# Kernel tuning notes

Measured on AMD Instinct MI355X. Metric: run time of the kernel, lower is better.

The kernel has to match this reference:

```python
import jax, jax.numpy as jnp
import numpy as np

# e2m1 (nvfp4) representable magnitudes and rounding midpoints
E2M1_POS = jnp.array([0.0, 0.5, 1.0, 1.5, 2.0, 3.0, 4.0, 6.0], dtype=jnp.float32)
E2M1_BOUNDS = jnp.array([0.25, 0.75, 1.25, 1.75, 2.5, 3.5, 5.0], dtype=jnp.float32)
E2M1_TABLE = jnp.concatenate([E2M1_POS, -E2M1_POS])  # 4-bit code -> value (sign bit = bit 3)
BLOCK = 16  # nvfp4 block-scale group size


def _fp8_round(v):
    # simulate storage of block scales in float8 e4m3
    return v.astype(jnp.float8_e4m3fn).astype(jnp.float32)


def _e2m1_round(v):
    # round-to-nearest onto the e2m1 grid (|v| must be pre-clipped to <= 6)
    idx = jnp.searchsorted(E2M1_BOUNDS, jnp.abs(v))
    return jnp.sign(v) * E2M1_POS[idx]


def setup_inputs() -> dict:
    key = jax.random.key(0)
    k1, k2, k3, k4, k5 = jax.random.split(key, 5)
    M, H = 4096, 4096
    x = jax.random.normal(k1, (M, 2 * H), dtype=jnp.float32)
    w = jax.random.randint(k2, (H, H // 2), 0, 256, dtype=jnp.int32)  # packed fp4, 2 nibbles/byte
    wscale = jax.random.normal(k3, (H, H // BLOCK), dtype=jnp.float32)  # cast to fp8 inside
    wscale2 = jax.random.uniform(k4, (1,), dtype=jnp.float32)
    scale = jax.random.uniform(k5, (1,), dtype=jnp.float32)
    return {"x": x, "w": w, "wscale": wscale, "wscale2": wscale2, "scale": scale}


def reference(x, w, wscale, wscale2, scale):
    M = x.shape[0]
    H = x.shape[1] // 2
    # SiLU-and-mul
    y = jax.nn.silu(x[:, :H]) * x[:, H:]                 # [M, H]
    gs = 1.0 / scale[0]                                  # global input scale (1/self.scale)
    # NVFP4 dynamic quant: per-16-element block amax -> fp8 block scale, values -> e2m1
    yb = y.reshape(M, H // BLOCK, BLOCK)
    amax = jnp.max(jnp.abs(yb), axis=-1)                 # [M, H/16]
    sf = _fp8_round(amax * (gs / 6.0))                   # fp8-stored block scales
    inv = jnp.where(sf > 0, gs / sf, 0.0)
    q = _e2m1_round(jnp.clip(yb * inv[..., None], -6.0, 6.0))
    a_deq = (q * sf[..., None]).reshape(M, H)            # fp4 value * fp8 block scale
    # Weight side: unpack fp4 nibbles (low nibble = even k), dequant with fp8 block scales
    wu = w.astype(jnp.uint8)
    lo = (wu & 0xF).astype(jnp.int32)
    hi = (wu >> 4).astype(jnp.int32)
    codes = jnp.stack([lo, hi], axis=-1).reshape(H, H)   # [N, K]
    b_q = E2M1_TABLE[codes]
    ws = _fp8_round(wscale)                              # model stores wscale in fp8
    b_deq = b_q * jnp.repeat(ws, BLOCK, axis=1)          # [N, K]
    # cutlass_scaled_fp4_mm with alpha = scale * wscale2 undoing global scales
    alpha = scale[0] * wscale2[0]
    out = alpha * (a_deq @ b_deq.T)                      # [M, N]
    return out
```

## Files before the change

kernel.cpp:

```cpp
#include <hip/hip_runtime.h>
#include <math.h>

typedef unsigned int uint;
typedef unsigned short ushort;
typedef __attribute__((ext_vector_type(8))) short bf16x8;
typedef __attribute__((ext_vector_type(4))) float f32x4;

static constexpr int Mdim = 4096;
static constexpr int Ndim = 4096;
static constexpr int Kdim = 4096;
static constexpr int Hdim = 4096;


__device__ __forceinline__ float fp8_round(float v) {
  float a = fabsf(v);
  float q;
  if (a >= 0x1p-6f) {
    uint u = __float_as_uint(a);
    int e = (int)(u >> 23) - 127;
    float quant = __uint_as_float((uint)(e - 3 + 127) << 23);
    q = rintf(a / quant) * quant;
    q = fminf(q, 448.f);
  } else {
    q = rintf(a * 512.f) * 0x1p-9f;
  }
  return copysignf(q, v);
}

__device__ __forceinline__ float e2m1_round(float t) {
  float a = fabsf(t);
  float q;
  if (a <= 0.25f) q = 0.f;
  else if (a <= 0.75f) q = 0.5f;
  else if (a <= 1.25f) q = 1.f;
  else if (a <= 1.75f) q = 1.5f;
  else if (a <= 2.5f)  q = 2.f;
  else if (a <= 3.5f)  q = 3.f;
  else if (a <= 5.f)   q = 4.f;
  else                 q = 6.f;
  return copysignf(q, t);
}

__device__ __forceinline__ float e2m1_decode(uint c) {
  uint m = c & 7u;
  float v;
  if (m == 0u) v = 0.f;
  else if (m == 1u) v = 0.5f;
  else v = __uint_as_float(((126u + (m >> 1)) << 23) | ((m & 1u) << 22));
  return (c & 8u) ? -v : v;
}


__global__ void silu_quant_kernel(const float* __restrict__ x, ushort* __restrict__ a_deq,
                                  const float* __restrict__ scalep) {
  const int g = blockIdx.x * 256 + threadIdx.x;
  const int row = g >> 8;
  const int blk = g & 255;
  const float gs = 1.0f / scalep[0];
  const float c6 = gs / 6.0f;
  const float* gp = x + (size_t)row * (2 * Hdim) + blk * 16;
  const float* up = gp + Hdim;
  float y[16];
  float amax = 0.f;
#pragma unroll
  for (int i = 0; i < 4; ++i) {
    float4 gv = ((const float4*)gp)[i];
    float4 uv = ((const float4*)up)[i];
    float ga[4] = {gv.x, gv.y, gv.z, gv.w};
    float ua[4] = {uv.x, uv.y, uv.z, uv.w};
#pragma unroll
    for (int j = 0; j < 4; ++j) {
      float xv = ga[j];
      float sig = 1.0f / (1.0f + expf(-xv));
      float yy = xv * sig * ua[j];
      y[i * 4 + j] = yy;
      amax = fmaxf(amax, fabsf(yy));
    }
  }
  const float sf = fp8_round(amax * c6);
  uint outp[8];
  if (sf > 0.f) {
    const float inv = gs / sf;
#pragma unroll
    for (int i = 0; i < 8; ++i) {
      float t0 = fminf(fmaxf(y[2 * i] * inv, -6.f), 6.f);
      float t1 = fminf(fmaxf(y[2 * i + 1] * inv, -6.f), 6.f);
      float d0 = e2m1_round(t0) * sf;
      float d1 = e2m1_round(t1) * sf;
      outp[i] = (__float_as_uint(d0) >> 16) | ((__float_as_uint(d1) >> 16) << 16);
    }
  } else {
#pragma unroll
    for (int i = 0; i < 8; ++i) outp[i] = 0u;
  }
  uint4* dst = (uint4*)(a_deq + (size_t)row * Hdim + blk * 16);
  dst[0] = (uint4){outp[0], outp[1], outp[2], outp[3]};
  dst[1] = (uint4){outp[4], outp[5], outp[6], outp[7]};
}


__global__ void wdeq_kernel(const int* __restrict__ w, const float* __restrict__ wscale,
                            ushort* __restrict__ b_deq) {
  const int g = blockIdx.x * 256 + threadIdx.x;
  const int n = g >> 8;
  const int blk = g & 255;
  const int4* wp = (const int4*)(w + (size_t)n * (Hdim / 2) + blk * 8);
  int4 w0 = wp[0], w1 = wp[1];
  int wb[8] = {w0.x, w0.y, w0.z, w0.w, w1.x, w1.y, w1.z, w1.w};
  const float ws = fp8_round(wscale[(size_t)n * (Hdim / 16) + blk]);
  uint outp[8];
#pragma unroll
  for (int i = 0; i < 8; ++i) {
    uint byte = (uint)wb[i] & 0xFFu;
    float vlo = e2m1_decode(byte & 15u) * ws;
    float vhi = e2m1_decode(byte >> 4) * ws;
    outp[i] = (__float_as_uint(vlo) >> 16) | ((__float_as_uint(vhi) >> 16) << 16);
  }
  uint4* dst = (uint4*)(b_deq + (size_t)n * Hdim + blk * 16);
  dst[0] = (uint4){outp[0], outp[1], outp[2], outp[3]};
  dst[1] = (uint4){outp[4], outp[5], outp[6], outp[7]};
}


#define BM 256
#define BN 256
#define BK 64
#define NT (Kdim / BK)
#define TILE_E (256 * 64)

__device__ __forceinline__ void gload_lds16(const ushort* g, ushort* l) {
  __builtin_amdgcn_global_load_lds((const __attribute__((address_space(1))) void*)g,
                                   (__attribute__((address_space(3))) void*)l,
                                   16, 0, 0);
}

#define STAGE(dst, mat, goff, h, kcol)                                        \
  do {                                                                        \
    gload_lds16((mat) + (size_t)goff[(h)*2 + 0] + (kcol), (dst) + loff[(h)*2 + 0]); \
    gload_lds16((mat) + (size_t)goff[(h)*2 + 1] + (kcol), (dst) + loff[(h)*2 + 1]); \
  } while (0)

__global__ __launch_bounds__(512, 2) void gemm256(const ushort* __restrict__ A,
                                                  const ushort* __restrict__ B,
                                                  float* __restrict__ C,
                                                  const float* __restrict__ scalep,
                                                  const float* __restrict__ wscale2p) {
  extern __shared__ __align__(16) ushort lds[];
  const int tid = threadIdx.x;
  const int wave = tid >> 6;
  const int lane = tid & 63;
  const int wm = wave >> 2;
  const int wn = wave & 3;
  const int fr = lane & 15;
  const int fq = lane >> 4;

  const int wg = blockIdx.x;
  const int swz = (wg & 7) * 32 + (wg >> 3);
  const int m0 = (swz >> 4) * BM;
  const int n0 = (swz & 15) * BN;

  f32x4 acc[8][4];
#pragma unroll
  for (int i = 0; i < 8; ++i)
#pragma unroll
    for (int j = 0; j < 4; ++j) acc[i][j] = (f32x4){0.f, 0.f, 0.f, 0.f};

  ushort* A0 = lds;
  ushort* A1 = lds + TILE_E;
  ushort* B0 = lds + 2 * TILE_E;
  ushort* B1 = lds + 3 * TILE_E;

  int goffA[4], goffB[4], loff[4];
#pragma unroll
  for (int h = 0; h < 2; ++h)
#pragma unroll
    for (int rr = 0; rr < 2; ++rr) {
      const int idx = h * 2 + rr;
      const int rowb = h * 128 + rr * 64 + wave * 8;
      const int trow = rowb + (lane >> 3);
      const int sc = (lane & 7) ^ (trow & 7);
      goffA[idx] = (m0 + trow) * Kdim + sc * 8;
      goffB[idx] = (n0 + trow) * Kdim + sc * 8;
      loff[idx] = rowb * 64;
    }

  const int laneAOff = (wm * 128 + fr) * 64;
  const int laneBOff = (wn * 64 + fr) * 64;
  const int xo0 = (fq ^ (fr & 7)) * 8;
  const int xo1 = ((4 + fq) ^ (fr & 7)) * 8;

  STAGE(A0, A, goffA, 0, 0);  STAGE(A0, A, goffA, 1, 0);
  STAGE(B0, B, goffB, 0, 0);  STAGE(B0, B, goffB, 1, 0);
  STAGE(B1, B, goffB, 0, BK); STAGE(B1, B, goffB, 1, BK);
  asm volatile("s_waitcnt vmcnt(4)" ::: "memory");
  __builtin_amdgcn_s_barrier();
  __builtin_amdgcn_sched_barrier(0);

#define MFMA_CLUSTER(base)                                                       \
  do {                                                                           \
    __builtin_amdgcn_s_setprio(1);                                               \
    _Pragma("unroll")                                                            \
    for (int m2 = 0; m2 < 2; ++m2)                                               \
      _Pragma("unroll")                                                          \
      for (int ni = 0; ni < 4; ++ni)                                             \
        _Pragma("unroll")                                                        \
        for (int kk = 0; kk < 2; ++kk)                                           \
          acc[(base) + m2][ni] = __builtin_amdgcn_mfma_f32_16x16x32_bf16(        \
              af[m2][kk], bfr[ni][kk], acc[(base) + m2][ni], 0, 0, 0);           \
    __builtin_amdgcn_s_setprio(0);                                               \
    __builtin_amdgcn_sched_barrier(0);                                           \
  } while (0)

  for (int u = 0; u < NT; ++u) {
    ushort* sA = (u & 1) ? A1 : A0;
    ushort* sB = (u & 1) ? B1 : B0;
    ushort* dA = (u & 1) ? A0 : A1;
    ushort* dB = sB;
    const int kA = (u + 1) * BK;
    const int kB = (u + 2) * BK;
    const bool gA = (u + 1) < NT;
    const bool gB = (u + 2) < NT;
    const ushort* aR0 = sA + laneAOff + xo0;
    const ushort* aR1 = sA + laneAOff + xo1;
    bf16x8 bfr[4][2], af[2][2];

    {
      const ushort* bR0 = sB + laneBOff + xo0;
      const ushort* bR1 = sB + laneBOff + xo1;
#pragma unroll
      for (int ni = 0; ni < 4; ++ni) {
        bfr[ni][0] = *(const bf16x8*)(bR0 + ni * 1024);
        bfr[ni][1] = *(const bf16x8*)(bR1 + ni * 1024);
      }
#pragma unroll
      for (int m2 = 0; m2 < 2; ++m2) {
        af[m2][0] = *(const bf16x8*)(aR0 + m2 * 1024);
        af[m2][1] = *(const bf16x8*)(aR1 + m2 * 1024);
      }
      if (gA) STAGE(dA, A, goffA, 0, kA);
      asm volatile("s_waitcnt lgkmcnt(8)" ::: "memory");
      __builtin_amdgcn_sched_barrier(0);
      __builtin_amdgcn_s_barrier();
      asm volatile("s_waitcnt lgkmcnt(0)" ::: "memory");
      __builtin_amdgcn_sched_barrier(0);
      MFMA_CLUSTER(0);
      __builtin_amdgcn_s_barrier();
      __builtin_amdgcn_sched_barrier(0);
    }
    {
#pragma unroll
      for (int m2 = 0; m2 < 2; ++m2) {
        af[m2][0] = *(const bf16x8*)(aR0 + (2 + m2) * 1024);
        af[m2][1] = *(const bf16x8*)(aR1 + (2 + m2) * 1024);
      }
      if (gA) STAGE(dA, A, goffA, 1, kA);
      __builtin_amdgcn_sched_barrier(0);
      __builtin_amdgcn_s_barrier();
      asm volatile("s_waitcnt lgkmcnt(0)" ::: "memory");
      __builtin_amdgcn_sched_barrier(0);
      MFMA_CLUSTER(2);
      __builtin_amdgcn_s_barrier();
      __builtin_amdgcn_sched_barrier(0);
    }
    {
#pragma unroll
      for (int m2 = 0; m2 < 2; ++m2) {
        af[m2][0] = *(const bf16x8*)(aR0 + (4 + m2) * 1024);
        af[m2][1] = *(const bf16x8*)(aR1 + (4 + m2) * 1024);
      }
      if (gB) STAGE(dB, B, goffB, 0, kB);
      __builtin_amdgcn_sched_barrier(0);
      __builtin_amdgcn_s_barrier();
      asm volatile("s_waitcnt lgkmcnt(0)" ::: "memory");
      __builtin_amdgcn_sched_barrier(0);
      MFMA_CLUSTER(4);
      __builtin_amdgcn_s_barrier();
      __builtin_amdgcn_sched_barrier(0);
    }
    {
#pragma unroll
      for (int m2 = 0; m2 < 2; ++m2) {
        af[m2][0] = *(const bf16x8*)(aR0 + (6 + m2) * 1024);
        af[m2][1] = *(const bf16x8*)(aR1 + (6 + m2) * 1024);
      }
      if (gB) STAGE(dB, B, goffB, 1, kB);
      __builtin_amdgcn_sched_barrier(0);
      __builtin_amdgcn_s_barrier();
      asm volatile("s_waitcnt lgkmcnt(0)" ::: "memory");
      __builtin_amdgcn_sched_barrier(0);
      MFMA_CLUSTER(6);
      if (gB) asm volatile("s_waitcnt vmcnt(4)" ::: "memory");
      else    asm volatile("s_waitcnt vmcnt(0)" ::: "memory");
      __builtin_amdgcn_s_barrier();
      __builtin_amdgcn_sched_barrier(0);
    }
  }

  const float alpha = scalep[0] * wscale2p[0];
#pragma unroll
  for (int mi = 0; mi < 8; ++mi)
#pragma unroll
    for (int ni = 0; ni < 4; ++ni) {
      const int col = n0 + wn * 64 + ni * 16 + fr;
      const int rbase = m0 + wm * 128 + mi * 16 + fq * 4;
#pragma unroll
      for (int r = 0; r < 4; ++r)
        C[(size_t)(rbase + r) * Ndim + col] = alpha * acc[mi][ni][r];
    }
}


extern "C" void kernel_launch(void* const* d_in, const int* in_sizes, int n_in,
                              void* d_out, int out_size, void* d_ws, size_t ws_size,
                              hipStream_t stream) {
  const float* x       = (const float*)d_in[0];
  const int*   w       = (const int*)d_in[1];
  const float* wscale  = (const float*)d_in[2];
  const float* wscale2 = (const float*)d_in[3];
  const float* scale   = (const float*)d_in[4];
  float* out = (float*)d_out;

  ushort* a_deq = (ushort*)d_ws;
  ushort* b_deq = a_deq + (size_t)Mdim * Kdim;

  silu_quant_kernel<<<Mdim, 256, 0, stream>>>(x, a_deq, scale);
  wdeq_kernel<<<Ndim, 256, 0, stream>>>(w, wscale, b_deq);

  hipFuncSetAttribute((const void*)gemm256, hipFuncAttributeMaxDynamicSharedMemorySize, 131072);
  gemm256<<<(Mdim / BM) * (Ndim / BN), 512, 131072, stream>>>(a_deq, b_deq, out, scale, wscale2);
}
```

Before: 168.0 us.

## Double-buffer A fragments across GEMM phases and prefetch next tile's first fragments

Reworks the GEMM main loop so A-operand register fragments ping-pong between two register sets. The first A fragments of the next K tile are loaded during the last phase of the current one, and the B stage for the next-next tile waits earlier with vmcnt(2). It also removes the sched_barrier after each MFMA cluster so the compiler can interleave more freely, and switches output stores to nontemporal. This aims to hide LDS read latency behind MFMAs, at the cost of more VGPRs and tighter ordering of the B buffer reuse.

```diff
diff --git a/kernel.cpp b/kernel.cpp
--- a/kernel.cpp
+++ b/kernel.cpp
@@ -134,10 +134,17 @@
                                    16, 0, 0);
 }
 
-#define STAGE(dst, mat, goff, h, kcol)                                        \
-  do {                                                                        \
+#define STAGE(dst, mat, goff, h, kcol)                                              \
+  do {                                                                              \
     gload_lds16((mat) + (size_t)goff[(h)*2 + 0] + (kcol), (dst) + loff[(h)*2 + 0]); \
     gload_lds16((mat) + (size_t)goff[(h)*2 + 1] + (kcol), (dst) + loff[(h)*2 + 1]); \
+  } while (0)
+
+#define BAR()                                   \
+  do {                                          \
+    asm volatile("" ::: "memory");              \
+    __builtin_amdgcn_s_barrier();               \
+    asm volatile("" ::: "memory");              \
   } while (0)
 
 __global__ __launch_bounds__(512, 2) void gemm256(const ushort* __restrict__ A,
@@ -165,10 +172,10 @@
 #pragma unroll
     for (int j = 0; j < 4; ++j) acc[i][j] = (f32x4){0.f, 0.f, 0.f, 0.f};
 
-  ushort* A0 = lds;
-  ushort* A1 = lds + TILE_E;
-  ushort* B0 = lds + 2 * TILE_E;
-  ushort* B1 = lds + 3 * TILE_E;
+  ushort* A0s = lds;
+  ushort* A1s = lds + TILE_E;
+  ushort* B0s = lds + 2 * TILE_E;
+  ushort* B1s = lds + 3 * TILE_E;
 
   int goffA[4], goffB[4], loff[4];
 #pragma unroll
@@ -189,14 +196,24 @@
   const int xo0 = (fq ^ (fr & 7)) * 8;
   const int xo1 = ((4 + fq) ^ (fr & 7)) * 8;
 
-  STAGE(A0, A, goffA, 0, 0);  STAGE(A0, A, goffA, 1, 0);
-  STAGE(B0, B, goffB, 0, 0);  STAGE(B0, B, goffB, 1, 0);
-  STAGE(B1, B, goffB, 0, BK); STAGE(B1, B, goffB, 1, BK);
+  STAGE(A0s, A, goffA, 0, 0);  STAGE(A0s, A, goffA, 1, 0);
+  STAGE(B0s, B, goffB, 0, 0);  STAGE(B0s, B, goffB, 1, 0);
+  STAGE(B1s, B, goffB, 0, BK); STAGE(B1s, B, goffB, 1, BK);
   asm volatile("s_waitcnt vmcnt(4)" ::: "memory");
-  __builtin_amdgcn_s_barrier();
-  __builtin_amdgcn_sched_barrier(0);
-
-#define MFMA_CLUSTER(base)                                                       \
+  BAR();
+
+  bf16x8 afA[2][2], afB[2][2], bfr[4][2];
+  {
+    const ushort* a0 = A0s + laneAOff + xo0;
+    const ushort* a1 = A0s + laneAOff + xo1;
+#pragma unroll
+    for (int m2 = 0; m2 < 2; ++m2) {
+      afB[m2][0] = *(const bf16x8*)(a0 + m2 * 1024);
+      afB[m2][1] = *(const bf16x8*)(a1 + m2 * 1024);
+    }
+  }
+
+#define MFMA_Q(base, af)                                                         \
   do {                                                                           \
     __builtin_amdgcn_s_setprio(1);                                               \
     _Pragma("unroll")                                                            \
@@ -208,21 +225,24 @@
           acc[(base) + m2][ni] = __builtin_amdgcn_mfma_f32_16x16x32_bf16(        \
               af[m2][kk], bfr[ni][kk], acc[(base) + m2][ni], 0, 0, 0);           \
     __builtin_amdgcn_s_setprio(0);                                               \
-    __builtin_amdgcn_sched_barrier(0);                                           \
   } while (0)
 
+#define LGKM0()                                          \
+  do {                                                   \
+    asm volatile("s_waitcnt lgkmcnt(0)" ::: "memory");   \
+    __builtin_amdgcn_sched_barrier(0);                   \
+  } while (0)
+
   for (int u = 0; u < NT; ++u) {
-    ushort* sA = (u & 1) ? A1 : A0;
-    ushort* sB = (u & 1) ? B1 : B0;
-    ushort* dA = (u & 1) ? A0 : A1;
-    ushort* dB = sB;
+    ushort* sA = (u & 1) ? A1s : A0s;
+    ushort* sB = (u & 1) ? B1s : B0s;
+    ushort* dA = (u & 1) ? A0s : A1s;
     const int kA = (u + 1) * BK;
     const int kB = (u + 2) * BK;
     const bool gA = (u + 1) < NT;
     const bool gB = (u + 2) < NT;
     const ushort* aR0 = sA + laneAOff + xo0;
     const ushort* aR1 = sA + laneAOff + xo1;
-    bf16x8 bfr[4][2], af[2][2];
 
     {
       const ushort* bR0 = sB + laneBOff + xo0;
@@ -232,67 +252,58 @@
         bfr[ni][0] = *(const bf16x8*)(bR0 + ni * 1024);
         bfr[ni][1] = *(const bf16x8*)(bR1 + ni * 1024);
       }
+      if (gA) STAGE(dA, A, goffA, 0, kA);
+      BAR();
+      LGKM0();
+      MFMA_Q(0, afB);
+      BAR();
+    }
+    {
 #pragma unroll
       for (int m2 = 0; m2 < 2; ++m2) {
-        af[m2][0] = *(const bf16x8*)(aR0 + m2 * 1024);
-        af[m2][1] = *(const bf16x8*)(aR1 + m2 * 1024);
-      }
-      if (gA) STAGE(dA, A, goffA, 0, kA);
-      asm volatile("s_waitcnt lgkmcnt(8)" ::: "memory");
-      __builtin_amdgcn_sched_barrier(0);
-      __builtin_amdgcn_s_barrier();
-      asm volatile("s_waitcnt lgkmcnt(0)" ::: "memory");
-      __builtin_amdgcn_sched_barrier(0);
-      MFMA_CLUSTER(0);
-      __builtin_amdgcn_s_barrier();
-      __builtin_amdgcn_sched_barrier(0);
+        afA[m2][0] = *(const bf16x8*)(aR0 + (2 + m2) * 1024);
+        afA[m2][1] = *(const bf16x8*)(aR1 + (2 + m2) * 1024);
+      }
+      if (gA) STAGE(dA, A, goffA, 1, kA);
+      BAR();
+      LGKM0();
+      MFMA_Q(2, afA);
+      BAR();
     }
     {
 #pragma unroll
       for (int m2 = 0; m2 < 2; ++m2) {
-        af[m2][0] = *(const bf16x8*)(aR0 + (2 + m2) * 1024);
-        af[m2][1] = *(const bf16x8*)(aR1 + (2 + m2) * 1024);
-      }
-      if (gA) STAGE(dA, A, goffA, 1, kA);
-      __builtin_amdgcn_sched_barrier(0);
-      __builtin_amdgcn_s_barrier();
-      asm volatile("s_waitcnt lgkmcnt(0)" ::: "memory");
-      __builtin_amdgcn_sched_barrier(0);
-      MFMA_CLUSTER(2);
-      __builtin_amdgcn_s_barrier();
-      __builtin_amdgcn_sched_barrier(0);
+        afB[m2][0] = *(const bf16x8*)(aR0 + (4 + m2) * 1024);
+        afB[m2][1] = *(const bf16x8*)(aR1 + (4 + m2) * 1024);
+      }
+      if (gB) STAGE(sB, B, goffB, 0, kB);
+      BAR();
+      LGKM0();
+      MFMA_Q(4, afB);
+      if (gB) asm volatile("s_waitcnt vmcnt(2)" ::: "memory");
+      else    asm volatile("s_waitcnt vmcnt(0)" ::: "memory");
+      BAR();
     }
     {
 #pragma unroll
       for (int m2 = 0; m2 < 2; ++m2) {
-        af[m2][0] = *(const bf16x8*)(aR0 + (4 + m2) * 1024);
-        af[m2][1] = *(const bf16x8*)(aR1 + (4 + m2) * 1024);
-      }
-      if (gB) STAGE(dB, B, goffB, 0, kB);
-      __builtin_amdgcn_sched_barrier(0);
-      __builtin_amdgcn_s_barrier();
-      asm volatile("s_waitcnt lgkmcnt(0)" ::: "memory");
-      __builtin_amdgcn_sched_barrier(0);
-      MFMA_CLUSTER(4);
-      __builtin_amdgcn_s_barrier();
-      __builtin_amdgcn_sched_barrier(0);
-    }
-    {
-#pragma unroll
-      for (int m2 = 0; m2 < 2; ++m2) {
-        af[m2][0] = *(const bf16x8*)(aR0 + (6 + m2) * 1024);
-        af[m2][1] = *(const bf16x8*)(aR1 + (6 + m2) * 1024);
-      }
-      if (gB) STAGE(dB, B, goffB, 1, kB);
-      __builtin_amdgcn_sched_barrier(0);
-      __builtin_amdgcn_s_barrier();
-      asm volatile("s_waitcnt lgkmcnt(0)" ::: "memory");
-      __builtin_amdgcn_sched_barrier(0);
-      MFMA_CLUSTER(6);
-      if (gB) asm volatile("s_waitcnt vmcnt(4)" ::: "memory");
-      else    asm volatile("s_waitcnt vmcnt(0)" ::: "memory");
-      __builtin_amdgcn_s_barrier();
-      __builtin_amdgcn_sched_barrier(0);
+        afA[m2][0] = *(const bf16x8*)(aR0 + (6 + m2) * 1024);
+        afA[m2][1] = *(const bf16x8*)(aR1 + (6 + m2) * 1024);
+      }
+      if (gA) {
+        const ushort* aN0 = dA + laneAOff + xo0;
+        const ushort* aN1 = dA + laneAOff + xo1;
+#pragma unroll
+        for (int m2 = 0; m2 < 2; ++m2) {
+          afB[m2][0] = *(const bf16x8*)(aN0 + m2 * 1024);
+          afB[m2][1] = *(const bf16x8*)(aN1 + m2 * 1024);
+        }
+      }
+      if (gB) STAGE(sB, B, goffB, 1, kB);
+      BAR();
+      LGKM0();
+      MFMA_Q(6, afA);
+      BAR();
     }
   }
 
@@ -305,7 +316,8 @@
       const int rbase = m0 + wm * 128 + mi * 16 + fq * 4;
 #pragma unroll
       for (int r = 0; r < 4; ++r)
-        C[(size_t)(rbase + r) * Ndim + col] = alpha * acc[mi][ni][r];
+        __builtin_nontemporal_store(alpha * acc[mi][ni][r],
+                                    &C[(size_t)(rbase + r) * Ndim + col]);
     }
 }
 
@@ -326,6 +338,6 @@
   silu_quant_kernel<<<Mdim, 256, 0, stream>>>(x, a_deq, scale);
   wdeq_kernel<<<Ndim, 256, 0, stream>>>(w, wscale, b_deq);
 
-  hipFuncSetAttribute((const void*)gemm256, hipFuncAttributeMaxDynamicSharedMemorySize, 131072);
+  (void)hipFuncSetAttribute((const void*)gemm256, hipFuncAttributeMaxDynamicSharedMemorySize, 131072);
   gemm256<<<(Mdim / BM) * (Ndim / BN), 512, 131072, stream>>>(a_deq, b_deq, out, scale, wscale2);
 }
```

After: 159.7 us. 1.05x faster.
